# Optimization experiments

Hardware: AMD Instinct MI355X
Metric: run time of the kernel (lower is better)

## Reference

```python
import jax, jax.numpy as jnp
import numpy as np

NUM_HEADS = 4
EPS = 1e-5


def conv1(W, b, z):
    # Conv1d with kernel_size=1 == channel-wise linear: (B, Cin, L) -> (B, Cout, L)
    return jnp.einsum('oi,bil->bol', W, z) + b[None, :, None]


def setup_inputs() -> dict:
    key = jax.random.key(0)
    ks = jax.random.split(key, 16)
    B, D, N = 2, 256, 4096
    s = 0.05
    return {
        'x': jax.random.normal(ks[0], (B, D, N), jnp.float32),
        'source': jax.random.normal(ks[1], (B, D, N), jnp.float32),
        'Wq': jax.random.normal(ks[2], (D, D), jnp.float32) * s,
        'bq': jax.random.normal(ks[3], (D,), jnp.float32) * s,
        'Wk': jax.random.normal(ks[4], (D, D), jnp.float32) * s,
        'bk': jax.random.normal(ks[5], (D,), jnp.float32) * s,
        'Wv': jax.random.normal(ks[6], (D, D), jnp.float32) * s,
        'bv': jax.random.normal(ks[7], (D,), jnp.float32) * s,
        'Wm': jax.random.normal(ks[8], (D, D), jnp.float32) * s,
        'bm': jax.random.normal(ks[9], (D,), jnp.float32) * s,
        'W1': jax.random.normal(ks[10], (2 * D, 2 * D), jnp.float32) * s,
        'b1': jax.random.normal(ks[11], (2 * D,), jnp.float32) * s,
        'W2': jax.random.normal(ks[12], (D, 2 * D), jnp.float32) * s,
        'b2': jax.random.normal(ks[13], (D,), jnp.float32) * s,
    }


def reference(x, source, Wq, bq, Wk, bk, Wv, bv, Wm, bm, W1, b1, W2, b2):
    B, D, N = x.shape
    M = source.shape[2]
    H = NUM_HEADS
    dim = D // H  # per-head dim; torch reshape splits channels as (dim, heads)

    q = conv1(Wq, bq, x).reshape(B, dim, H, N)
    k = conv1(Wk, bk, source).reshape(B, dim, H, M)
    v = conv1(Wv, bv, source).reshape(B, dim, H, M)

    scores = jnp.einsum('bdhn,bdhm->bhnm', q, k) / (dim ** 0.5)
    prob = jax.nn.softmax(scores, axis=-1)
    attn = jnp.einsum('bhnm,bdhm->bdhn', prob, v).reshape(B, D, N)

    message = conv1(Wm, bm, attn)

    h = conv1(W1, b1, jnp.concatenate([x, message], axis=1))
    # InstanceNorm1d (affine=False, biased var over L)
    mu = jnp.mean(h, axis=2, keepdims=True)
    var = jnp.mean((h - mu) ** 2, axis=2, keepdims=True)
    h = jax.nn.relu((h - mu) / jnp.sqrt(var + EPS))
    return conv1(W2, b2, h)
```

## Files before the change

kernel.cpp:

```cpp
#include <hip/hip_runtime.h>
#include <cstdint>
#include <cstddef>


typedef __attribute__((ext_vector_type(8))) short short8;
typedef __attribute__((ext_vector_type(4))) float floatx4;

__device__ __forceinline__ unsigned short f2bf(float x) {
  union { float f; unsigned int u; } c; c.f = x;
  unsigned int r = c.u + 0x7FFFu + ((c.u >> 16) & 1u);
  return (unsigned short)(r >> 16);
}
__device__ __forceinline__ float bf2f(unsigned short u) {
  union { unsigned int i; float f; } c; c.i = ((unsigned int)u) << 16; return c.f;
}

__global__ __launch_bounds__(256) void tx_kernel(
    const float* __restrict__ X, unsigned short* __restrict__ Y, int C, int N)
{
  __shared__ float tile[32][33];
  const int n0 = blockIdx.x * 32, c0 = blockIdx.y * 32, b = blockIdx.z;
  const int tc = threadIdx.x & 31, tr = threadIdx.x >> 5;
  #pragma unroll
  for (int i = 0; i < 4; ++i) {
    const int c = c0 + tr + i * 8;
    tile[tr + i * 8][tc] = X[((size_t)b * C + c) * N + n0 + tc];
  }
  __syncthreads();
  #pragma unroll
  for (int i = 0; i < 4; ++i) {
    const int n = n0 + tr + i * 8;
    Y[((size_t)b * N + n) * C + c0 + tc] = f2bf(tile[tc][tr + i * 8]);
  }
}

__global__ __launch_bounds__(256) void wconv(
    const float* __restrict__ src, unsigned short* __restrict__ dst,
    int Co, int Ci, int permR, int permC, float scale)
{
  const int idx = blockIdx.x * 256 + threadIdx.x;
  if (idx >= Co * Ci) return;
  const int op = idx / Ci, ip = idx % Ci;
  const int o = permR ? 4 * (op & 63) + (op >> 6) : op;
  const int i = permC ? 4 * (ip & 63) + (ip >> 6) : ip;
  dst[idx] = f2bf(src[(size_t)o * Ci + i] * scale);
}

__global__ __launch_bounds__(256) void bconv(
    const float* __restrict__ bq, const float* __restrict__ bk,
    const float* __restrict__ bv, const float* __restrict__ bm,
    const float* __restrict__ b1, const float* __restrict__ b2,
    float* __restrict__ dst)
{
  const int t = blockIdx.x * 256 + threadIdx.x;
  if (t < 256)       dst[t] = bq[4 * (t & 63) + (t >> 6)] * 0.1803368801111137f;
  else if (t < 512)  { const int z = t - 256; dst[t] = bk[4 * (z & 63) + (z >> 6)]; }
  else if (t < 768)  { const int z = t - 512; dst[t] = bv[4 * (z & 63) + (z >> 6)]; }
  else if (t < 1024) dst[t] = bm[t - 768];
  else if (t < 1536) dst[t] = b1[t - 1024];
  else if (t < 1792) dst[t] = b2[t - 1536];
}

__global__ __launch_bounds__(256) void gemm128(
    const unsigned short* __restrict__ Wb, const float* __restrict__ bias,
    const unsigned short* __restrict__ X0, const unsigned short* __restrict__ X1,
    void* __restrict__ O0, void* __restrict__ O1, void* __restrict__ O2,
    int Co, int Ci, int Ci0, int N, int variant)
{
  const int n0 = blockIdx.x * 128;
  const int o0 = blockIdx.y * 128;
  const int b  = blockIdx.z;
  const int t  = threadIdx.x;
  const int w = t >> 6, lane = t & 63, qd = lane >> 4, l = lane & 15;
  const int oh = (w >> 1) * 64, nh = (w & 1) * 64;

  __shared__ unsigned short Wl[128 * 64];
  __shared__ unsigned short Xl[128 * 64];

  floatx4 acc[4][4];
  #pragma unroll
  for (int i = 0; i < 4; ++i)
    #pragma unroll
    for (int j = 0; j < 4; ++j) acc[i][j] = (floatx4){0.f, 0.f, 0.f, 0.f};

  for (int k0 = 0; k0 < Ci; k0 += 64) {
    const unsigned short* Xs; int cb, rl;
    if (variant == 1) { Xs = (o0 < 256) ? X0 : X1; cb = k0; rl = Ci; }
    else if (k0 < Ci0) { Xs = X0; cb = k0; rl = Ci0; }
    else               { Xs = X1; cb = k0 - Ci0; rl = Ci - Ci0; }
    __syncthreads();
    #pragma unroll
    for (int i = 0; i < 4; ++i) {
      const int idx = i * 256 + t;
      const int row = idx >> 3, pg = idx & 7;
      const int ph = (pg ^ (row & 7)) * 8;
      *(short8*)&Wl[row * 64 + ph] =
          *(const short8*)&Wb[(size_t)(o0 + row) * Ci + k0 + pg * 8];
      *(short8*)&Xl[row * 64 + ph] =
          *(const short8*)&Xs[((size_t)b * N + n0 + row) * rl + cb + pg * 8];
    }
    __syncthreads();

    short8 af[4][2], bf[4][2];
    #pragma unroll
    for (int i = 0; i < 4; ++i) {
      const int ar = oh + 16 * i + l;
      af[i][0] = *(const short8*)&Wl[ar * 64 + ((qd ^ (ar & 7))) * 8];
      af[i][1] = *(const short8*)&Wl[ar * 64 + (((4 + qd) ^ (ar & 7))) * 8];
    }
    #pragma unroll
    for (int j = 0; j < 4; ++j) {
      const int br = nh + 16 * j + l;
      bf[j][0] = *(const short8*)&Xl[br * 64 + ((qd ^ (br & 7))) * 8];
      bf[j][1] = *(const short8*)&Xl[br * 64 + (((4 + qd) ^ (br & 7))) * 8];
    }
    #pragma unroll
    for (int i = 0; i < 4; ++i)
      #pragma unroll
      for (int j = 0; j < 4; ++j) {
        acc[i][j] = __builtin_amdgcn_mfma_f32_16x16x32_bf16(af[i][0], bf[j][0], acc[i][j], 0, 0, 0);
        acc[i][j] = __builtin_amdgcn_mfma_f32_16x16x32_bf16(af[i][1], bf[j][1], acc[i][j], 0, 0, 0);
      }
  }

  const int osec = o0 + oh;
  #pragma unroll
  for (int i = 0; i < 4; ++i) {
    const int o4 = o0 + oh + 16 * i + qd * 4;
    const float4 bi = *(const float4*)&bias[o4];
    #pragma unroll
    for (int j = 0; j < 4; ++j) {
      const int n = n0 + nh + 16 * j + l;
      if (variant == 0) {
        unsigned short* C = (unsigned short*)O0;
        ushort4 pk;
        pk.x = f2bf(acc[i][j][0] + bi.x); pk.y = f2bf(acc[i][j][1] + bi.y);
        pk.z = f2bf(acc[i][j][2] + bi.z); pk.w = f2bf(acc[i][j][3] + bi.w);
        *(ushort4*)&C[((size_t)b * N + n) * Co + o4] = pk;
      } else if (variant == 1) {
        if (osec < 256) {
          unsigned short* C = (unsigned short*)O0;
          ushort4 pk;
          pk.x = f2bf(acc[i][j][0] + bi.x); pk.y = f2bf(acc[i][j][1] + bi.y);
          pk.z = f2bf(acc[i][j][2] + bi.z); pk.w = f2bf(acc[i][j][3] + bi.w);
          *(ushort4*)&C[((size_t)b * N + n) * 256 + o4] = pk;
        } else if (osec < 512) {
          unsigned short* C = (unsigned short*)O1;
          ushort4 pk;
          pk.x = f2bf(acc[i][j][0] + bi.x); pk.y = f2bf(acc[i][j][1] + bi.y);
          pk.z = f2bf(acc[i][j][2] + bi.z); pk.w = f2bf(acc[i][j][3] + bi.w);
          *(ushort4*)&C[((size_t)b * N + n) * 256 + (o4 - 256)] = pk;
        } else {
          unsigned short* C = (unsigned short*)O2;
          #pragma unroll
          for (int rg = 0; rg < 4; ++rg) {
            const int op = o4 - 512 + rg, h = op >> 6, d = op & 63;
            C[(((size_t)b * 4 + h) * 64 + d) * N + n] =
                f2bf(acc[i][j][rg] + ((const float*)&bi)[rg]);
          }
        }
      } else {
        float* C = (float*)O0;
        #pragma unroll
        for (int rg = 0; rg < 4; ++rg)
          C[((size_t)b * Co + o4 + rg) * N + n] = acc[i][j][rg] + ((const float*)&bi)[rg];
      }
    }
  }
}

__global__ __launch_bounds__(256) void attn_mfma(
    const unsigned short* __restrict__ qb, const unsigned short* __restrict__ kb,
    const unsigned short* __restrict__ vh, unsigned short* __restrict__ ob,
    int N)
{
  const int n0 = blockIdx.x * 64;
  const int h  = blockIdx.y;
  const int b  = blockIdx.z;
  const int t  = threadIdx.x;
  const int w = t >> 6, lane = t & 63, qd = lane >> 4, l = lane & 15;

  __shared__ unsigned short Kl[64 * 64];
  __shared__ unsigned short Vl[64 * 64];
  __shared__ unsigned short Pl[4][16 * 64];

  const int qrow = n0 + 16 * w + l;
  const unsigned short* qp = &qb[((size_t)b * N + qrow) * 256 + h * 64];
  const short8 aQ0 = *(const short8*)&qp[qd * 8];
  const short8 aQ1 = *(const short8*)&qp[32 + qd * 8];

  floatx4 accO[4];
  #pragma unroll
  for (int ds = 0; ds < 4; ++ds) accO[ds] = (floatx4){0.f, 0.f, 0.f, 0.f};
  float li[4] = {0.f, 0.f, 0.f, 0.f};

  for (int j0 = 0; j0 < N; j0 += 64) {
    __syncthreads();
    #pragma unroll
    for (int i = 0; i < 2; ++i) {
      const int idx = i * 256 + t;
      const int row = idx >> 3, pg = idx & 7;
      const int ph = (pg ^ (row & 7)) * 8;
      *(short8*)&Kl[row * 64 + ph] =
          *(const short8*)&kb[((size_t)b * N + j0 + row) * 256 + h * 64 + pg * 8];
      *(short8*)&Vl[row * 64 + ph] =
          *(const short8*)&vh[(((size_t)b * 4 + h) * 64 + row) * N + j0 + pg * 8];
    }
    __syncthreads();

    floatx4 S[4];
    #pragma unroll
    for (int js = 0; js < 4; ++js) {
      const int br = 16 * js + l;
      const short8 b0 = *(const short8*)&Kl[br * 64 + ((qd ^ (br & 7))) * 8];
      const short8 b1 = *(const short8*)&Kl[br * 64 + (((4 + qd) ^ (br & 7))) * 8];
      floatx4 a = (floatx4){0.f, 0.f, 0.f, 0.f};
      a = __builtin_amdgcn_mfma_f32_16x16x32_bf16(aQ0, b0, a, 0, 0, 0);
      a = __builtin_amdgcn_mfma_f32_16x16x32_bf16(aQ1, b1, a, 0, 0, 0);
      S[js] = a;
    }

    #pragma unroll
    for (int js = 0; js < 4; ++js) {
      const int kg = 2 * js + (l >> 3);
      #pragma unroll
      for (int rg = 0; rg < 4; ++rg) {
        const float p = __builtin_exp2f(S[js][rg]);
        li[rg] += p;
        union { float f; unsigned int u; } cv; cv.f = p;
        const int qr = qd * 4 + rg;
        Pl[w][qr * 64 + ((kg ^ (qr & 7))) * 8 + (l & 7)] =
            (unsigned short)((cv.u + 0x8000u) >> 16);
      }
    }

    const short8 aP0 = *(const short8*)&Pl[w][l * 64 + ((qd ^ (l & 7))) * 8];
    const short8 aP1 = *(const short8*)&Pl[w][l * 64 + (((4 + qd) ^ (l & 7))) * 8];
    #pragma unroll
    for (int ds = 0; ds < 4; ++ds) {
      const int br = 16 * ds + l;
      const short8 b0 = *(const short8*)&Vl[br * 64 + ((qd ^ (br & 7))) * 8];
      const short8 b1 = *(const short8*)&Vl[br * 64 + (((4 + qd) ^ (br & 7))) * 8];
      accO[ds] = __builtin_amdgcn_mfma_f32_16x16x32_bf16(aP0, b0, accO[ds], 0, 0, 0);
      accO[ds] = __builtin_amdgcn_mfma_f32_16x16x32_bf16(aP1, b1, accO[ds], 0, 0, 0);
    }
  }

  #pragma unroll
  for (int rg = 0; rg < 4; ++rg) {
    float s = li[rg];
    s += __shfl_xor(s, 1);
    s += __shfl_xor(s, 2);
    s += __shfl_xor(s, 4);
    s += __shfl_xor(s, 8);
    const float inv = 1.f / s;
    const int nq = n0 + 16 * w + qd * 4 + rg;
    #pragma unroll
    for (int ds = 0; ds < 4; ++ds)
      ob[((size_t)b * N + nq) * 256 + h * 64 + 16 * ds + l] =
          f2bf(accO[ds][rg] * inv);
  }
}

__global__ __launch_bounds__(256) void in_stats(
    const unsigned short* __restrict__ H, float* __restrict__ Ps,
    float* __restrict__ Ps2, int N)
{
  const int cg = blockIdx.x, ns = blockIdx.y, b = blockIdx.z, t = threadIdx.x;
  const int c0 = cg * 64 + (t & 7) * 8;
  float s[8] = {}, s2[8] = {};
  #pragma unroll
  for (int i = 0; i < 8; ++i) {
    const int n = ns * 256 + (t >> 3) + i * 32;
    const short8 hv = *(const short8*)&H[((size_t)b * N + n) * 512 + c0];
    #pragma unroll
    for (int j = 0; j < 8; ++j) {
      const float f = bf2f((unsigned short)hv[j]);
      s[j] += f; s2[j] += f * f;
    }
  }
  __shared__ float rs[32][64], rs2[32][64];
  #pragma unroll
  for (int j = 0; j < 8; ++j) {
    rs[t >> 3][(t & 7) * 8 + j] = s[j];
    rs2[t >> 3][(t & 7) * 8 + j] = s2[j];
  }
  __syncthreads();
  if (t < 64) {
    float a = 0.f, a2 = 0.f;
    #pragma unroll
    for (int r = 0; r < 32; ++r) { a += rs[r][t]; a2 += rs2[r][t]; }
    const size_t o = ((size_t)ns * 2 + b) * 512 + cg * 64 + t;
    Ps[o] = a; Ps2[o] = a2;
  }
}

__global__ __launch_bounds__(256) void in_final(
    const float* __restrict__ Ps, const float* __restrict__ Ps2,
    float* __restrict__ Mu, float* __restrict__ Inv, int N)
{
  const int idx = blockIdx.x * 256 + threadIdx.x;
  if (idx >= 1024) return;
  const int b = idx >> 9, c = idx & 511;
  float s = 0.f, s2 = 0.f;
  for (int ns = 0; ns < 16; ++ns) {
    s  += Ps [((size_t)ns * 2 + b) * 512 + c];
    s2 += Ps2[((size_t)ns * 2 + b) * 512 + c];
  }
  const float mu = s / (float)N;
  const float var = fmaxf(s2 / (float)N - mu * mu, 0.f);
  Mu[idx] = mu;
  Inv[idx] = rsqrtf(var + 1e-5f);
}

__global__ __launch_bounds__(256) void in_norm(
    unsigned short* __restrict__ H, const float* __restrict__ Mu,
    const float* __restrict__ Inv, int N)
{
  const int cg = blockIdx.x, ns = blockIdx.y, b = blockIdx.z, t = threadIdx.x;
  const int c0 = cg * 64 + (t & 7) * 8;
  float mu[8], iv[8];
  #pragma unroll
  for (int j = 0; j < 8; ++j) {
    mu[j] = Mu[b * 512 + c0 + j];
    iv[j] = Inv[b * 512 + c0 + j];
  }
  #pragma unroll
  for (int i = 0; i < 8; ++i) {
    const int n = ns * 256 + (t >> 3) + i * 32;
    unsigned short* p = (unsigned short*)&H[((size_t)b * N + n) * 512 + c0];
    short8 hv = *(const short8*)p;
    #pragma unroll
    for (int j = 0; j < 8; ++j) {
      const float f = fmaxf((bf2f((unsigned short)hv[j]) - mu[j]) * iv[j], 0.f);
      hv[j] = (short)f2bf(f);
    }
    *(short8*)p = hv;
  }
}

extern "C" void kernel_launch(void* const* d_in, const int* in_sizes, int n_in,
                              void* d_out, int out_size, void* d_ws, size_t ws_size,
                              hipStream_t stream)
{
  const int B = 2, D = 256, N = 4096;

  const float* x   = (const float*)d_in[0];
  const float* src = (const float*)d_in[1];
  const float* Wq  = (const float*)d_in[2];  const float* bq = (const float*)d_in[3];
  const float* Wk  = (const float*)d_in[4];  const float* bk = (const float*)d_in[5];
  const float* Wv  = (const float*)d_in[6];  const float* bv = (const float*)d_in[7];
  const float* Wm  = (const float*)d_in[8];  const float* bm = (const float*)d_in[9];
  const float* W1  = (const float*)d_in[10]; const float* b1 = (const float*)d_in[11];
  const float* W2  = (const float*)d_in[12]; const float* b2 = (const float*)d_in[13];
  float* out = (float*)d_out;

  char* ws = (char*)d_ws;
  const size_t MB = 1u << 20;
  unsigned short* xb  = (unsigned short*)(ws + 0 * MB);
  unsigned short* sb  = (unsigned short*)(ws + 4 * MB);
  unsigned short* qbf = (unsigned short*)(ws + 8 * MB);
  unsigned short* kbf = (unsigned short*)(ws + 12 * MB);
  unsigned short* vhb = (unsigned short*)(ws + 16 * MB);
  unsigned short* atb = (unsigned short*)(ws + 20 * MB);
  unsigned short* msb = (unsigned short*)(ws + 24 * MB);
  unsigned short* hb  = (unsigned short*)(ws + 28 * MB);
  unsigned short* wqkvb = (unsigned short*)(ws + 36 * MB);
  unsigned short* wmb = wqkvb + 768 * 256;
  unsigned short* w1b = wmb + 256 * 256;
  unsigned short* w2b = w1b + 512 * 512;
  float* biasb = (float*)(ws + 38 * MB);
  float* Ps    = biasb + 2048;
  float* Ps2   = Ps + 16 * 2 * 512;
  float* Mu    = Ps2 + 16 * 2 * 512;
  float* Inv   = Mu + 1024;

  const dim3 blk(256);

  tx_kernel<<<dim3(N / 32, D / 32, B), blk, 0, stream>>>(x,   xb, D, N);
  tx_kernel<<<dim3(N / 32, D / 32, B), blk, 0, stream>>>(src, sb, D, N);
  wconv<<<dim3(256), blk, 0, stream>>>(Wq, wqkvb,             256, 256, 1, 0, 0.1803368801111137f);
  wconv<<<dim3(256), blk, 0, stream>>>(Wk, wqkvb + 256 * 256, 256, 256, 1, 0, 1.f);
  wconv<<<dim3(256), blk, 0, stream>>>(Wv, wqkvb + 512 * 256, 256, 256, 1, 0, 1.f);
  wconv<<<dim3(256), blk, 0, stream>>>(Wm, wmb, 256, 256, 0, 1, 1.f);
  wconv<<<dim3(1024), blk, 0, stream>>>(W1, w1b, 512, 512, 0, 0, 1.f);
  wconv<<<dim3(512), blk, 0, stream>>>(W2, w2b, 256, 512, 0, 0, 1.f);
  bconv<<<dim3(7), blk, 0, stream>>>(bq, bk, bv, bm, b1, b2, biasb);

  gemm128<<<dim3(N / 128, 6, B), blk, 0, stream>>>(
      wqkvb, biasb, xb, sb, qbf, kbf, vhb, 768, 256, 256, N, 1);

  attn_mfma<<<dim3(N / 64, 4, B), blk, 0, stream>>>(qbf, kbf, vhb, atb, N);

  gemm128<<<dim3(N / 128, 2, B), blk, 0, stream>>>(
      wmb, biasb + 768, atb, atb, msb, nullptr, nullptr, 256, 256, 256, N, 0);

  gemm128<<<dim3(N / 128, 4, B), blk, 0, stream>>>(
      w1b, biasb + 1024, xb, msb, hb, nullptr, nullptr, 512, 512, 256, N, 0);

  in_stats<<<dim3(8, 16, B), blk, 0, stream>>>(hb, Ps, Ps2, N);
  in_final<<<dim3(4), blk, 0, stream>>>(Ps, Ps2, Mu, Inv, N);
  in_norm<<<dim3(8, 16, B), blk, 0, stream>>>(hb, Mu, Inv, N);

  gemm128<<<dim3(N / 128, 2, B), blk, 0, stream>>>(
      w2b, biasb + 1536, hb, hb, out, nullptr, nullptr, 256, 512, 512, N, 2);
}
```

Before: 253.4 us.

## Split attention over key ranges, use direct-to-LDS loads, fuse prep kernels

The attention kernel now splits the key dimension four ways. Each block handles 128 queries and reuses the K/V fragments held in registers across two query sub-tiles, writing partial outputs and row sums that a new combine kernel reduces and normalizes. Global-to-shared copies in the GEMM and attention kernels switch to global_load_lds with the swizzle moved onto the source address. The transpose, weight-conversion and bias kernels are merged into two launches, and the instance-norm finalize step is folded into the normalize kernel. This cuts launch count and raises attention parallelism and reuse, at the cost of extra partial-output traffic and a bf16 rounding of the partial sums.

Measured after the change: 233.5 us. -7.8%, faster.

```diff
diff --git a/kernel.cpp b/kernel.cpp
--- a/kernel.cpp
+++ b/kernel.cpp
@@ -14,51 +14,74 @@
 __device__ __forceinline__ float bf2f(unsigned short u) {
   union { unsigned int i; float f; } c; c.i = ((unsigned int)u) << 16; return c.f;
 }
-
-__global__ __launch_bounds__(256) void tx_kernel(
-    const float* __restrict__ X, unsigned short* __restrict__ Y, int C, int N)
+__device__ __forceinline__ void gload16(const void* g, void* l) {
+  __builtin_amdgcn_global_load_lds(
+      (const __attribute__((address_space(1))) unsigned int*)g,
+      (__attribute__((address_space(3))) unsigned int*)l, 16, 0, 0);
+}
+
+#define LOG2E_8 0.18033688011112042f
+
+__global__ __launch_bounds__(256) void tx_all(
+    const float* __restrict__ x, const float* __restrict__ src,
+    unsigned short* __restrict__ xb, unsigned short* __restrict__ sb,
+    int C, int N)
 {
   __shared__ float tile[32][33];
-  const int n0 = blockIdx.x * 32, c0 = blockIdx.y * 32, b = blockIdx.z;
+  const int which = blockIdx.z >> 1, b = blockIdx.z & 1;
+  const float* X = which ? src : x;
+  unsigned short* Y = which ? sb : xb;
+  const int n0 = blockIdx.x * 32, c0 = blockIdx.y * 32;
   const int tc = threadIdx.x & 31, tr = threadIdx.x >> 5;
   #pragma unroll
-  for (int i = 0; i < 4; ++i) {
-    const int c = c0 + tr + i * 8;
-    tile[tr + i * 8][tc] = X[((size_t)b * C + c) * N + n0 + tc];
-  }
+  for (int i = 0; i < 4; ++i)
+    tile[tr + i * 8][tc] = X[((size_t)b * C + c0 + tr + i * 8) * N + n0 + tc];
   __syncthreads();
   #pragma unroll
-  for (int i = 0; i < 4; ++i) {
-    const int n = n0 + tr + i * 8;
-    Y[((size_t)b * N + n) * C + c0 + tc] = f2bf(tile[tc][tr + i * 8]);
-  }
-}
-
-__global__ __launch_bounds__(256) void wconv(
-    const float* __restrict__ src, unsigned short* __restrict__ dst,
-    int Co, int Ci, int permR, int permC, float scale)
-{
-  const int idx = blockIdx.x * 256 + threadIdx.x;
-  if (idx >= Co * Ci) return;
-  const int op = idx / Ci, ip = idx % Ci;
-  const int o = permR ? 4 * (op & 63) + (op >> 6) : op;
-  const int i = permC ? 4 * (ip & 63) + (ip >> 6) : ip;
-  dst[idx] = f2bf(src[(size_t)o * Ci + i] * scale);
-}
-
-__global__ __launch_bounds__(256) void bconv(
+  for (int i = 0; i < 4; ++i)
+    Y[((size_t)b * N + n0 + tr + i * 8) * C + c0 + tc] = f2bf(tile[tc][tr + i * 8]);
+}
+
+__global__ __launch_bounds__(256) void wprep(
+    const float* __restrict__ Wq, const float* __restrict__ Wk,
+    const float* __restrict__ Wv, const float* __restrict__ Wm,
+    const float* __restrict__ W1, const float* __restrict__ W2,
     const float* __restrict__ bq, const float* __restrict__ bk,
     const float* __restrict__ bv, const float* __restrict__ bm,
     const float* __restrict__ b1, const float* __restrict__ b2,
-    float* __restrict__ dst)
-{
-  const int t = blockIdx.x * 256 + threadIdx.x;
-  if (t < 256)       dst[t] = bq[4 * (t & 63) + (t >> 6)] * 0.1803368801111137f;
-  else if (t < 512)  { const int z = t - 256; dst[t] = bk[4 * (z & 63) + (z >> 6)]; }
-  else if (t < 768)  { const int z = t - 512; dst[t] = bv[4 * (z & 63) + (z >> 6)]; }
-  else if (t < 1024) dst[t] = bm[t - 768];
-  else if (t < 1536) dst[t] = b1[t - 1024];
-  else if (t < 1792) dst[t] = b2[t - 1536];
+    unsigned short* __restrict__ wqkv, unsigned short* __restrict__ wm_,
+    unsigned short* __restrict__ w1_, unsigned short* __restrict__ w2_,
+    float* __restrict__ biasb)
+{
+  const int bid = blockIdx.x, t = threadIdx.x;
+  if (bid < 768) {
+    const int idx = bid * 256 + t;
+    const int op = idx >> 8, ip = idx & 255;
+    const int grp = op >> 8, oo = op & 255;
+    const int o = 4 * (oo & 63) + (oo >> 6);
+    const float* W = grp == 0 ? Wq : grp == 1 ? Wk : Wv;
+    const float sc = grp == 0 ? LOG2E_8 : 1.f;
+    wqkv[idx] = f2bf(W[(size_t)o * 256 + ip] * sc);
+  } else if (bid < 1024) {
+    const int idx = (bid - 768) * 256 + t;
+    const int op = idx >> 8, ip = idx & 255;
+    const int i2 = 4 * (ip & 63) + (ip >> 6);
+    wm_[idx] = f2bf(Wm[(size_t)op * 256 + i2]);
+  } else if (bid < 2048) {
+    const int idx = (bid - 1024) * 256 + t;
+    w1_[idx] = f2bf(W1[idx]);
+  } else if (bid < 2560) {
+    const int idx = (bid - 2048) * 256 + t;
+    w2_[idx] = f2bf(W2[idx]);
+  } else {
+    const int z = (bid - 2560) * 256 + t;
+    if (z < 256)       biasb[z] = bq[4 * (z & 63) + (z >> 6)] * LOG2E_8;
+    else if (z < 512)  { const int y = z - 256; biasb[z] = bk[4 * (y & 63) + (y >> 6)]; }
+    else if (z < 768)  { const int y = z - 512; biasb[z] = bv[4 * (y & 63) + (y >> 6)]; }
+    else if (z < 1024) biasb[z] = bm[z - 768];
+    else if (z < 1536) biasb[z] = b1[z - 1024];
+    else if (z < 1792) biasb[z] = b2[z - 1536];
+  }
 }
 
 __global__ __launch_bounds__(256) void gemm128(
@@ -92,12 +115,9 @@
     #pragma unroll
     for (int i = 0; i < 4; ++i) {
       const int idx = i * 256 + t;
-      const int row = idx >> 3, pg = idx & 7;
-      const int ph = (pg ^ (row & 7)) * 8;
-      *(short8*)&Wl[row * 64 + ph] =
-          *(const short8*)&Wb[(size_t)(o0 + row) * Ci + k0 + pg * 8];
-      *(short8*)&Xl[row * 64 + ph] =
-          *(const short8*)&Xs[((size_t)b * N + n0 + row) * rl + cb + pg * 8];
+      const int row = idx >> 3, pg = idx & 7, sg = pg ^ (row & 7);
+      gload16(&Wb[(size_t)(o0 + row) * Ci + k0 + sg * 8], &Wl[row * 64 + pg * 8]);
+      gload16(&Xs[((size_t)b * N + n0 + row) * rl + cb + sg * 8], &Xl[row * 64 + pg * 8]);
     }
     __syncthreads();
 
@@ -171,12 +191,13 @@
 
 __global__ __launch_bounds__(256) void attn_mfma(
     const unsigned short* __restrict__ qb, const unsigned short* __restrict__ kb,
-    const unsigned short* __restrict__ vh, unsigned short* __restrict__ ob,
-    int N)
-{
-  const int n0 = blockIdx.x * 64;
+    const unsigned short* __restrict__ vh, unsigned short* __restrict__ Opart,
+    float* __restrict__ liPart, int N)
+{
+  const int qt = blockIdx.x;
   const int h  = blockIdx.y;
-  const int b  = blockIdx.z;
+  const int b  = blockIdx.z >> 2, s = blockIdx.z & 3;
+  const int n0 = qt * 128;
   const int t  = threadIdx.x;
   const int w = t >> 6, lane = t & 63, qd = lane >> 4, l = lane & 15;
 
@@ -184,81 +205,136 @@
   __shared__ unsigned short Vl[64 * 64];
   __shared__ unsigned short Pl[4][16 * 64];
 
-  const int qrow = n0 + 16 * w + l;
-  const unsigned short* qp = &qb[((size_t)b * N + qrow) * 256 + h * 64];
-  const short8 aQ0 = *(const short8*)&qp[qd * 8];
-  const short8 aQ1 = *(const short8*)&qp[32 + qd * 8];
-
-  floatx4 accO[4];
-  #pragma unroll
-  for (int ds = 0; ds < 4; ++ds) accO[ds] = (floatx4){0.f, 0.f, 0.f, 0.f};
-  float li[4] = {0.f, 0.f, 0.f, 0.f};
-
-  for (int j0 = 0; j0 < N; j0 += 64) {
+  const unsigned short* qp0 = &qb[((size_t)b * N + n0 + 16 * w + l) * 256 + h * 64];
+  const unsigned short* qp1 = qp0 + (size_t)64 * 256;
+  short8 aQ[2][2];
+  aQ[0][0] = *(const short8*)&qp0[qd * 8];
+  aQ[0][1] = *(const short8*)&qp0[32 + qd * 8];
+  aQ[1][0] = *(const short8*)&qp1[qd * 8];
+  aQ[1][1] = *(const short8*)&qp1[32 + qd * 8];
+
+  floatx4 accO[2][4];
+  #pragma unroll
+  for (int qs = 0; qs < 2; ++qs)
+    #pragma unroll
+    for (int ds = 0; ds < 4; ++ds) accO[qs][ds] = (floatx4){0.f, 0.f, 0.f, 0.f};
+  float li[2][4] = {};
+
+  const int j0base = s * 1024;
+  for (int jt = 0; jt < 16; ++jt) {
+    const int j0 = j0base + jt * 64;
     __syncthreads();
     #pragma unroll
     for (int i = 0; i < 2; ++i) {
       const int idx = i * 256 + t;
-      const int row = idx >> 3, pg = idx & 7;
-      const int ph = (pg ^ (row & 7)) * 8;
-      *(short8*)&Kl[row * 64 + ph] =
-          *(const short8*)&kb[((size_t)b * N + j0 + row) * 256 + h * 64 + pg * 8];
-      *(short8*)&Vl[row * 64 + ph] =
-          *(const short8*)&vh[(((size_t)b * 4 + h) * 64 + row) * N + j0 + pg * 8];
+      const int row = idx >> 3, pg = idx & 7, sg = pg ^ (row & 7);
+      gload16(&kb[((size_t)b * N + j0 + row) * 256 + h * 64 + sg * 8],
+              &Kl[row * 64 + pg * 8]);
+      gload16(&vh[(((size_t)b * 4 + h) * 64 + row) * N + j0 + sg * 8],
+              &Vl[row * 64 + pg * 8]);
     }
     __syncthreads();
 
-    floatx4 S[4];
+    short8 kf[4][2], vf[4][2];
     #pragma unroll
     for (int js = 0; js < 4; ++js) {
       const int br = 16 * js + l;
-      const short8 b0 = *(const short8*)&Kl[br * 64 + ((qd ^ (br & 7))) * 8];
-      const short8 b1 = *(const short8*)&Kl[br * 64 + (((4 + qd) ^ (br & 7))) * 8];
-      floatx4 a = (floatx4){0.f, 0.f, 0.f, 0.f};
-      a = __builtin_amdgcn_mfma_f32_16x16x32_bf16(aQ0, b0, a, 0, 0, 0);
-      a = __builtin_amdgcn_mfma_f32_16x16x32_bf16(aQ1, b1, a, 0, 0, 0);
-      S[js] = a;
-    }
-
-    #pragma unroll
-    for (int js = 0; js < 4; ++js) {
-      const int kg = 2 * js + (l >> 3);
-      #pragma unroll
-      for (int rg = 0; rg < 4; ++rg) {
-        const float p = __builtin_exp2f(S[js][rg]);
-        li[rg] += p;
-        union { float f; unsigned int u; } cv; cv.f = p;
-        const int qr = qd * 4 + rg;
-        Pl[w][qr * 64 + ((kg ^ (qr & 7))) * 8 + (l & 7)] =
-            (unsigned short)((cv.u + 0x8000u) >> 16);
+      kf[js][0] = *(const short8*)&Kl[br * 64 + ((qd ^ (br & 7))) * 8];
+      kf[js][1] = *(const short8*)&Kl[br * 64 + (((4 + qd) ^ (br & 7))) * 8];
+      vf[js][0] = *(const short8*)&Vl[br * 64 + ((qd ^ (br & 7))) * 8];
+      vf[js][1] = *(const short8*)&Vl[br * 64 + (((4 + qd) ^ (br & 7))) * 8];
+    }
+
+    #pragma unroll
+    for (int qs = 0; qs < 2; ++qs) {
+      floatx4 S[4];
+      #pragma unroll
+      for (int js = 0; js < 4; ++js) {
+        floatx4 a = (floatx4){0.f, 0.f, 0.f, 0.f};
+        a = __builtin_amdgcn_mfma_f32_16x16x32_bf16(aQ[qs][0], kf[js][0], a, 0, 0, 0);
+        a = __builtin_amdgcn_mfma_f32_16x16x32_bf16(aQ[qs][1], kf[js][1], a, 0, 0, 0);
+        S[js] = a;
       }
-    }
-
-    const short8 aP0 = *(const short8*)&Pl[w][l * 64 + ((qd ^ (l & 7))) * 8];
-    const short8 aP1 = *(const short8*)&Pl[w][l * 64 + (((4 + qd) ^ (l & 7))) * 8];
-    #pragma unroll
-    for (int ds = 0; ds < 4; ++ds) {
-      const int br = 16 * ds + l;
-      const short8 b0 = *(const short8*)&Vl[br * 64 + ((qd ^ (br & 7))) * 8];
-      const short8 b1 = *(const short8*)&Vl[br * 64 + (((4 + qd) ^ (br & 7))) * 8];
-      accO[ds] = __builtin_amdgcn_mfma_f32_16x16x32_bf16(aP0, b0, accO[ds], 0, 0, 0);
-      accO[ds] = __builtin_amdgcn_mfma_f32_16x16x32_bf16(aP1, b1, accO[ds], 0, 0, 0);
-    }
-  }
-
-  #pragma unroll
-  for (int rg = 0; rg < 4; ++rg) {
-    float s = li[rg];
-    s += __shfl_xor(s, 1);
-    s += __shfl_xor(s, 2);
-    s += __shfl_xor(s, 4);
-    s += __shfl_xor(s, 8);
-    const float inv = 1.f / s;
-    const int nq = n0 + 16 * w + qd * 4 + rg;
-    #pragma unroll
-    for (int ds = 0; ds < 4; ++ds)
-      ob[((size_t)b * N + nq) * 256 + h * 64 + 16 * ds + l] =
-          f2bf(accO[ds][rg] * inv);
+      #pragma unroll
+      for (int js = 0; js < 4; ++js) {
+        const int kg = 2 * js + (l >> 3);
+        #pragma unroll
+        for (int rg = 0; rg < 4; ++rg) {
+          const float p = __builtin_exp2f(S[js][rg]);
+          li[qs][rg] += p;
+          union { float f; unsigned int u; } cv; cv.f = p;
+          const int qr = qd * 4 + rg;
+          Pl[w][qr * 64 + ((kg ^ (qr & 7))) * 8 + (l & 7)] =
+              (unsigned short)((cv.u + 0x8000u) >> 16);
+        }
+      }
+      const short8 aP0 = *(const short8*)&Pl[w][l * 64 + ((qd ^ (l & 7))) * 8];
+      const short8 aP1 = *(const short8*)&Pl[w][l * 64 + (((4 + qd) ^ (l & 7))) * 8];
+      #pragma unroll
+      for (int ds = 0; ds < 4; ++ds) {
+        accO[qs][ds] = __builtin_amdgcn_mfma_f32_16x16x32_bf16(aP0, vf[ds][0], accO[qs][ds], 0, 0, 0);
+        accO[qs][ds] = __builtin_amdgcn_mfma_f32_16x16x32_bf16(aP1, vf[ds][1], accO[qs][ds], 0, 0, 0);
+      }
+    }
+  }
+
+  const size_t obase = ((((size_t)b * 4 + h) * 4 + s) * 32 + qt) * 128;
+  #pragma unroll
+  for (int qs = 0; qs < 2; ++qs)
+    #pragma unroll
+    for (int rg = 0; rg < 4; ++rg) {
+      float sum = li[qs][rg];
+      sum += __shfl_xor(sum, 1);
+      sum += __shfl_xor(sum, 2);
+      sum += __shfl_xor(sum, 4);
+      sum += __shfl_xor(sum, 8);
+      const int q = qs * 64 + 16 * w + qd * 4 + rg;
+      #pragma unroll
+      for (int ds = 0; ds < 4; ++ds)
+        Opart[(obase + q) * 64 + 16 * ds + l] = f2bf(accO[qs][ds][rg]);
+      if (l == 0) liPart[obase + q] = sum;
+    }
+}
+
+__global__ __launch_bounds__(256) void attn_combine(
+    const unsigned short* __restrict__ Opart, const float* __restrict__ liPart,
+    unsigned short* __restrict__ atb, int N)
+{
+  const int qt = blockIdx.x, h = blockIdx.y, b = blockIdx.z;
+  const int t = threadIdx.x;
+  const int q = t >> 1, d0 = (t & 1) * 32;
+
+  float li = 0.f;
+  size_t idx[4];
+  #pragma unroll
+  for (int s = 0; s < 4; ++s) {
+    idx[s] = ((((size_t)b * 4 + h) * 4 + s) * 32 + qt) * 128 + q;
+    li += liPart[idx[s]];
+  }
+  const float inv = 1.f / li;
+
+  float o[32];
+  #pragma unroll
+  for (int c = 0; c < 32; ++c) o[c] = 0.f;
+  #pragma unroll
+  for (int s = 0; s < 4; ++s) {
+    #pragma unroll
+    for (int c4 = 0; c4 < 4; ++c4) {
+      const short8 v = *(const short8*)&Opart[idx[s] * 64 + d0 + c4 * 8];
+      #pragma unroll
+      for (int j = 0; j < 8; ++j) o[c4 * 8 + j] += bf2f((unsigned short)v[j]);
+    }
+  }
+  unsigned short* dst = &atb[((size_t)b * N + qt * 128 + q) * 256 + h * 64 + d0];
+  #pragma unroll
+  for (int c4 = 0; c4 < 4; ++c4) {
+    ushort4 pk;
+    pk.x = f2bf(o[c4 * 8 + 0] * inv); pk.y = f2bf(o[c4 * 8 + 1] * inv);
+    pk.z = f2bf(o[c4 * 8 + 2] * inv); pk.w = f2bf(o[c4 * 8 + 3] * inv);
+    *(ushort4*)&dst[c4 * 8] = pk;
+    pk.x = f2bf(o[c4 * 8 + 4] * inv); pk.y = f2bf(o[c4 * 8 + 5] * inv);
+    pk.z = f2bf(o[c4 * 8 + 6] * inv); pk.w = f2bf(o[c4 * 8 + 7] * inv);
+    *(ushort4*)&dst[c4 * 8 + 4] = pk;
   }
 }
 
@@ -295,40 +371,36 @@
   }
 }
 
-__global__ __launch_bounds__(256) void in_final(
-    const float* __restrict__ Ps, const float* __restrict__ Ps2,
-    float* __restrict__ Mu, float* __restrict__ Inv, int N)
-{
-  const int idx = blockIdx.x * 256 + threadIdx.x;
-  if (idx >= 1024) return;
-  const int b = idx >> 9, c = idx & 511;
-  float s = 0.f, s2 = 0.f;
-  for (int ns = 0; ns < 16; ++ns) {
-    s  += Ps [((size_t)ns * 2 + b) * 512 + c];
-    s2 += Ps2[((size_t)ns * 2 + b) * 512 + c];
-  }
-  const float mu = s / (float)N;
-  const float var = fmaxf(s2 / (float)N - mu * mu, 0.f);
-  Mu[idx] = mu;
-  Inv[idx] = rsqrtf(var + 1e-5f);
-}
-
 __global__ __launch_bounds__(256) void in_norm(
-    unsigned short* __restrict__ H, const float* __restrict__ Mu,
-    const float* __restrict__ Inv, int N)
+    unsigned short* __restrict__ H, const float* __restrict__ Ps,
+    const float* __restrict__ Ps2, int N)
 {
   const int cg = blockIdx.x, ns = blockIdx.y, b = blockIdx.z, t = threadIdx.x;
+  __shared__ float muS[64], ivS[64];
+  if (t < 64) {
+    const int c = cg * 64 + t;
+    float s = 0.f, s2 = 0.f;
+    for (int k = 0; k < 16; ++k) {
+      s  += Ps [((size_t)k * 2 + b) * 512 + c];
+      s2 += Ps2[((size_t)k * 2 + b) * 512 + c];
+    }
+    const float mu = s / (float)N;
+    const float var = fmaxf(s2 / (float)N - mu * mu, 0.f);
+    muS[t] = mu;
+    ivS[t] = rsqrtf(var + 1e-5f);
+  }
+  __syncthreads();
   const int c0 = cg * 64 + (t & 7) * 8;
   float mu[8], iv[8];
   #pragma unroll
   for (int j = 0; j < 8; ++j) {
-    mu[j] = Mu[b * 512 + c0 + j];
-    iv[j] = Inv[b * 512 + c0 + j];
+    mu[j] = muS[(t & 7) * 8 + j];
+    iv[j] = ivS[(t & 7) * 8 + j];
   }
   #pragma unroll
   for (int i = 0; i < 8; ++i) {
     const int n = ns * 256 + (t >> 3) + i * 32;
-    unsigned short* p = (unsigned short*)&H[((size_t)b * N + n) * 512 + c0];
+    unsigned short* p = &H[((size_t)b * N + n) * 512 + c0];
     short8 hv = *(const short8*)p;
     #pragma unroll
     for (int j = 0; j < 8; ++j) {
@@ -363,34 +435,31 @@
   unsigned short* kbf = (unsigned short*)(ws + 12 * MB);
   unsigned short* vhb = (unsigned short*)(ws + 16 * MB);
   unsigned short* atb = (unsigned short*)(ws + 20 * MB);
+  unsigned short* Opart = (unsigned short*)(ws + 24 * MB);
   unsigned short* msb = (unsigned short*)(ws + 24 * MB);
   unsigned short* hb  = (unsigned short*)(ws + 28 * MB);
-  unsigned short* wqkvb = (unsigned short*)(ws + 36 * MB);
+  float* liPart = (float*)(ws + 41 * MB);
+  unsigned short* wqkvb = (unsigned short*)(ws + 42 * MB);
   unsigned short* wmb = wqkvb + 768 * 256;
   unsigned short* w1b = wmb + 256 * 256;
   unsigned short* w2b = w1b + 512 * 512;
-  float* biasb = (float*)(ws + 38 * MB);
+  float* biasb = (float*)(ws + 44 * MB);
   float* Ps    = biasb + 2048;
   float* Ps2   = Ps + 16 * 2 * 512;
-  float* Mu    = Ps2 + 16 * 2 * 512;
-  float* Inv   = Mu + 1024;
 
   const dim3 blk(256);
 
-  tx_kernel<<<dim3(N / 32, D / 32, B), blk, 0, stream>>>(x,   xb, D, N);
-  tx_kernel<<<dim3(N / 32, D / 32, B), blk, 0, stream>>>(src, sb, D, N);
-  wconv<<<dim3(256), blk, 0, stream>>>(Wq, wqkvb,             256, 256, 1, 0, 0.1803368801111137f);
-  wconv<<<dim3(256), blk, 0, stream>>>(Wk, wqkvb + 256 * 256, 256, 256, 1, 0, 1.f);
-  wconv<<<dim3(256), blk, 0, stream>>>(Wv, wqkvb + 512 * 256, 256, 256, 1, 0, 1.f);
-  wconv<<<dim3(256), blk, 0, stream>>>(Wm, wmb, 256, 256, 0, 1, 1.f);
-  wconv<<<dim3(1024), blk, 0, stream>>>(W1, w1b, 512, 512, 0, 0, 1.f);
-  wconv<<<dim3(512), blk, 0, stream>>>(W2, w2b, 256, 512, 0, 0, 1.f);
-  bconv<<<dim3(7), blk, 0, stream>>>(bq, bk, bv, bm, b1, b2, biasb);
+  tx_all<<<dim3(N / 32, D / 32, 2 * B), blk, 0, stream>>>(x, src, xb, sb, D, N);
+  wprep<<<dim3(2567), blk, 0, stream>>>(Wq, Wk, Wv, Wm, W1, W2,
+                                        bq, bk, bv, bm, b1, b2,
+                                        wqkvb, wmb, w1b, w2b, biasb);
 
   gemm128<<<dim3(N / 128, 6, B), blk, 0, stream>>>(
       wqkvb, biasb, xb, sb, qbf, kbf, vhb, 768, 256, 256, N, 1);
 
-  attn_mfma<<<dim3(N / 64, 4, B), blk, 0, stream>>>(qbf, kbf, vhb, atb, N);
+  attn_mfma<<<dim3(N / 128, 4, B * 4), blk, 0, stream>>>(
+      qbf, kbf, vhb, Opart, liPart, N);
+  attn_combine<<<dim3(N / 128, 4, B), blk, 0, stream>>>(Opart, liPart, atb, N);
 
   gemm128<<<dim3(N / 128, 2, B), blk, 0, stream>>>(
       wmb, biasb + 768, atb, atb, msb, nullptr, nullptr, 256, 256, 256, N, 0);
@@ -399,8 +468,7 @@
       w1b, biasb + 1024, xb, msb, hb, nullptr, nullptr, 512, 512, 256, N, 0);
 
   in_stats<<<dim3(8, 16, B), blk, 0, stream>>>(hb, Ps, Ps2, N);
-  in_final<<<dim3(4), blk, 0, stream>>>(Ps, Ps2, Mu, Inv, N);
-  in_norm<<<dim3(8, 16, B), blk, 0, stream>>>(hb, Mu, Inv, N);
+  in_norm<<<dim3(8, 16, B), blk, 0, stream>>>(hb, Ps, Ps2, N);
 
   gemm128<<<dim3(N / 128, 2, B), blk, 0, stream>>>(
       w2b, biasb + 1536, hb, hb, out, nullptr, nullptr, 256, 512, 512, N, 2);
```
